# Kernel tuning notes

Measured on AMD Instinct MI355X. Metric: run time of the kernel, lower is better.

## Reference

```python
import jax, jax.numpy as jnp
import numpy as np

B, NN, F, H = 8, 1024, 256, 8
D = F // H
SCALE = D ** -0.5


def setup_inputs() -> dict:
    key = jax.random.key(0)
    ks = jax.random.split(key, 12)
    s = 0.02
    inp = {
        'ndata': jax.random.normal(ks[0], (B, NN, F), jnp.float32),
        'N': NN,
        'attn_bias': jax.random.normal(ks[1], (B, NN, NN, H), jnp.float32),
        'attn_mask': jax.random.randint(ks[2], (B, NN, NN), 0, 2).astype(bool),
        'Wq': jax.random.normal(ks[3], (F, F), jnp.float32) * s,
        'bq': jnp.zeros((F,), jnp.float32),
        'Wk': jax.random.normal(ks[4], (F, F), jnp.float32) * s,
        'bk': jnp.zeros((F,), jnp.float32),
        'Wv': jax.random.normal(ks[5], (F, F), jnp.float32) * s,
        'bv': jnp.zeros((F,), jnp.float32),
        'Wo': jax.random.normal(ks[6], (F, F), jnp.float32) * s,
        'bo': jnp.zeros((F,), jnp.float32),
    }
    return inp


def reference(ndata, N, attn_bias, attn_mask, Wq, bq, Wk, bk, Wv, bv, Wo, bo):
    b, n, f = ndata.shape
    # QKV projections (torch nn.Linear: x @ W.T + b), split heads
    q = (ndata @ Wq.T + bq).reshape(b, n, H, D) * SCALE
    k = (ndata @ Wk.T + bk).reshape(b, n, H, D)
    v = (ndata @ Wv.T + bv).reshape(b, n, H, D)
    # scores: (b, q, k, h) matching torch layout after its transposes
    scores = jnp.einsum('bqhd,bkhd->bqkh', q, k)
    scores = scores + attn_bias  # additive bias
    # original code force-unmasks column 0 so every row has a valid entry
    mask = attn_mask.at[:, :, 0].set(False)
    scores = jnp.where(mask[..., None], -jnp.inf, scores)
    attn = jax.nn.softmax(scores, axis=2)  # softmax over keys
    out = jnp.einsum('bqkh,bkhd->bqhd', attn, v).reshape(b, n, f)
    return out @ Wo.T + bo
```

## Files before the change

### kernel.cpp

```cpp
#include <hip/hip_runtime.h>
#include <hip/hip_bf16.h>

typedef __attribute__((ext_vector_type(8))) short short8;
typedef __attribute__((ext_vector_type(4))) float f32x4;

#define MFMA16(a,b,c) __builtin_amdgcn_mfma_f32_16x16x32_bf16((a),(b),(c),0,0,0)

static __device__ __forceinline__ unsigned int f2bf(float f){
    unsigned int u = __float_as_uint(f);
    u += 0x7FFFu + ((u >> 16) & 1u);
    return u >> 16;
}

static __device__ __forceinline__ short8 pack8(float4 a, float4 b){
    short8 r;
    r[0]=(short)f2bf(a.x); r[1]=(short)f2bf(a.y);
    r[2]=(short)f2bf(a.z); r[3]=(short)f2bf(a.w);
    r[4]=(short)f2bf(b.x); r[5]=(short)f2bf(b.y);
    r[6]=(short)f2bf(b.z); r[7]=(short)f2bf(b.w);
    return r;
}

__global__ __launch_bounds__(256) void mask_prep_k(
    const unsigned int* __restrict__ m, unsigned int* __restrict__ bmout)
{
    __shared__ int any_hi;
    const int tid  = threadIdx.x;
    const int lane = tid & 63;
    const unsigned int gbase = blockIdx.x*256u + tid;
    if (tid == 0) any_hi = 0;

    unsigned int wv[8]; unsigned int acc = 0;
    #pragma unroll
    for (int it = 0; it < 8; ++it){
        wv[it] = m[it*262144u + gbase];
        acc |= wv[it];
    }
    __syncthreads();
    if (acc & 0xFFFFFF00u) atomicOr(&any_hi, 1);
    __syncthreads();

    if (any_hi == 0){
        for (int it = 0; it < 32; ++it){
            unsigned int idx = it*262144u + gbase;
            unsigned int v = m[idx];
            unsigned long long bal = __ballot(v != 0u);
            if (lane == 0)
                *(unsigned long long*)(bmout + (idx >> 5)) = bal;
        }
    } else {
        #pragma unroll
        for (int it = 0; it < 8; ++it){
            unsigned int idx = it*262144u + gbase;
            unsigned int v = wv[it];
            unsigned int nib = (v | (v>>7) | (v>>14) | (v>>21)) & 0xFu;
            unsigned int x = nib << ((lane & 7)*4);
            x |= (unsigned int)__shfl_xor((int)x, 1);
            x |= (unsigned int)__shfl_xor((int)x, 2);
            x |= (unsigned int)__shfl_xor((int)x, 4);
            if ((lane & 7) == 0)
                bmout[idx >> 3] = x;
        }
    }
}

__global__ __launch_bounds__(256) void qkv_proj_k(
    const float* __restrict__ nd,
    const float* __restrict__ Wqp, const float* __restrict__ bqp,
    const float* __restrict__ Wkp, const float* __restrict__ bkp,
    const float* __restrict__ Wvp, const float* __restrict__ bvp,
    unsigned short* __restrict__ qout, unsigned short* __restrict__ kout,
    unsigned short* __restrict__ vtout)
{
    __shared__ __align__(16) unsigned short xl[64*264];
    const int tid  = threadIdx.x;
    const int bi   = blockIdx.x;
    const int kind = bi >> 7;
    const int R0   = (bi & 127) * 64;
    const int b    = R0 >> 10;
    const int n0   = R0 & 1023;

    #pragma unroll
    for (int it = 0; it < 16; ++it){
        int f4 = it*256 + tid;
        int r = f4 >> 6, c4 = f4 & 63;
        float4 v = *(const float4*)(nd + (size_t)(R0+r)*256 + c4*4);
        unsigned int lo = f2bf(v.x) | (f2bf(v.y) << 16);
        unsigned int hi = f2bf(v.z) | (f2bf(v.w) << 16);
        *(uint2*)&xl[r*264 + c4*4] = make_uint2(lo, hi);
    }
    __syncthreads();

    const int lane = tid & 63;
    const int w  = tid >> 6;
    const int ln = lane & 15;
    const int g  = lane >> 4;
    const int ow = w * 64;

    f32x4 acc[4][4];
    #pragma unroll
    for (int a=0;a<4;++a){
        #pragma unroll
        for (int c=0;c<4;++c) acc[a][c] = (f32x4){0.f,0.f,0.f,0.f};
    }

    if (kind < 2){
        const float* W  = kind ? Wkp : Wqp;
        const float* bb = kind ? bkp : bqp;
        unsigned short* op = kind ? kout : qout;
        const float scl = kind ? 1.0f : 0.17677669529663687f;
        for (int kk = 0; kk < 8; ++kk){
            short8 wf[4], xf[4];
            #pragma unroll
            for (int ot=0; ot<4; ++ot){
                const float* wp = W + (size_t)(ow + ot*16 + ln)*256 + kk*32 + g*8;
                wf[ot] = pack8(*(const float4*)wp, *(const float4*)(wp+4));
            }
            #pragma unroll
            for (int nt=0; nt<4; ++nt)
                xf[nt] = *(const short8*)&xl[(nt*16+ln)*264 + kk*32 + g*8];
            #pragma unroll
            for (int ot=0; ot<4; ++ot){
                #pragma unroll
                for (int nt=0; nt<4; ++nt)
                    acc[ot][nt] = MFMA16(wf[ot], xf[nt], acc[ot][nt]);
            }
        }
        #pragma unroll
        for (int ot=0; ot<4; ++ot){
            int o0 = ow + ot*16 + g*4;
            int h = o0 >> 5, d0 = o0 & 31;
            float4 b4 = *(const float4*)(bb + o0);
            #pragma unroll
            for (int nt=0; nt<4; ++nt){
                int n = n0 + nt*16 + ln;
                unsigned int lo = f2bf((acc[ot][nt][0]+b4.x)*scl) | (f2bf((acc[ot][nt][1]+b4.y)*scl)<<16);
                unsigned int hi = f2bf((acc[ot][nt][2]+b4.z)*scl) | (f2bf((acc[ot][nt][3]+b4.w)*scl)<<16);
                *(uint2*)(op + ((size_t)(b*8+h)*1024 + n)*32 + d0) = make_uint2(lo,hi);
            }
        }
    } else {
        for (int kk = 0; kk < 8; ++kk){
            short8 wf[4], xf[4];
            #pragma unroll
            for (int ot=0; ot<4; ++ot){
                const float* wp = Wvp + (size_t)(ow + ot*16 + ln)*256 + kk*32 + g*8;
                wf[ot] = pack8(*(const float4*)wp, *(const float4*)(wp+4));
            }
            #pragma unroll
            for (int nt=0; nt<4; ++nt)
                xf[nt] = *(const short8*)&xl[(nt*16+ln)*264 + kk*32 + g*8];
            #pragma unroll
            for (int nt=0; nt<4; ++nt){
                #pragma unroll
                for (int ot=0; ot<4; ++ot)
                    acc[nt][ot] = MFMA16(xf[nt], wf[ot], acc[nt][ot]);
            }
        }
        #pragma unroll
        for (int nt=0; nt<4; ++nt){
            int nb = n0 + nt*16 + g*4;
            #pragma unroll
            for (int ot=0; ot<4; ++ot){
                int o = ow + ot*16 + ln;
                int h = o >> 5, d = o & 31;
                float bvv = bvp[o];
                unsigned int lo = f2bf(acc[nt][ot][0]+bvv) | (f2bf(acc[nt][ot][1]+bvv)<<16);
                unsigned int hi = f2bf(acc[nt][ot][2]+bvv) | (f2bf(acc[nt][ot][3]+bvv)<<16);
                *(uint2*)(vtout + ((size_t)(b*8+h)*32 + d)*1024 + nb) = make_uint2(lo,hi);
            }
        }
    }
}

__global__ __launch_bounds__(256, 4) void attn_k(
    const unsigned short* __restrict__ qbuf, const unsigned short* __restrict__ kbuf,
    const unsigned short* __restrict__ vtbuf, const float* __restrict__ bias,
    const unsigned int* __restrict__ bm, unsigned short* __restrict__ ab)
{
    __shared__ __align__(16) float bs[4352];
    const int tid  = threadIdx.x;
    const int bi   = blockIdx.x;
    const int hh   = bi >> 9;
    const int b    = (bi >> 6) & 7;
    const int q0   = (bi & 63) * 16;
    const int lane = tid & 63;
    const int w    = tid >> 6;
    const int ln   = lane & 15;
    const int g    = lane >> 4;
    const int h    = hh*4 + w;

    const short8 qf = *(const short8*)(qbuf + ((size_t)(b*8+h)*1024 + q0 + ln)*32 + g*8);

    const int kperm = ((ln >> 2) << 3) + (ln & 3);
    const unsigned short* kp = kbuf  + ((size_t)(b*8+h)*1024 + kperm)*32 + g*8;
    const unsigned short* vp = vtbuf + ((size_t)(b*8+h)*32   + ln)*1024 + g*8;
    const unsigned int*  bmp = bm + (size_t)(b*1024 + q0 + ln)*32;

    const int sq  = tid >> 4;
    const int sk  = tid & 15;
    const float* bgp = bias + (size_t)(b*1024 + q0 + sq)*8192 + sk*8 + hh*4;
    const int hqb = sq*68;
    const int rb0 = w*1088 + ln*68 + 8*g;

    f32x4 acc0 = (f32x4){0.f,0.f,0.f,0.f};
    f32x4 acc1 = (f32x4){0.f,0.f,0.f,0.f};
    float lsum = 0.f;
    const f32x4 z4 = {0.f,0.f,0.f,0.f};

    float4 br0, br1, br2, br3;
    short8 kn0, kn1, kn2, kn3;
    unsigned int bm0, bm1;

#define LOAD_ALL(cc) do { int c_ = (cc); \
    br0 = *(const float4*)(bgp + (size_t)c_*512); \
    br1 = *(const float4*)(bgp + (size_t)c_*512 + 128); \
    br2 = *(const float4*)(bgp + (size_t)c_*512 + 256); \
    br3 = *(const float4*)(bgp + (size_t)c_*512 + 384); \
    kn0 = *(const short8*)(kp + c_*2048); \
    kn1 = *(const short8*)(kp + c_*2048 + 128); \
    kn2 = *(const short8*)(kp + c_*2048 + 1024); \
    kn3 = *(const short8*)(kp + c_*2048 + 1152); \
    bm0 = bmp[2*c_]; bm1 = bmp[2*c_+1]; } while(0)

#define STAGE1(R, IT) do { int kw_ = hqb + (IT)*16 + sk; \
    bs[kw_       ] = R.x; \
    bs[kw_ + 1088] = R.y; \
    bs[kw_ + 2176] = R.z; \
    bs[kw_ + 3264] = R.w; } while(0)

#define CHUNK_HALF(K0, K1, BMW, KH, VOFF) do { \
    f32x4 s0 = MFMA16(K0, qf, z4);    \
    f32x4 s1 = MFMA16(K1, qf, z4);    \
    f32x4 blo = *(const f32x4*)&bs[rb0 + (KH)*32]; \
    f32x4 bhi = *(const f32x4*)&bs[rb0 + (KH)*32 + 4]; \
    short8 vf0 = *(const short8*)(vp + (VOFF)); \
    short8 vf1 = *(const short8*)(vp + (VOFF) + 16*1024); \
    unsigned int mb_ = (BMW) >> (g*8); \
    float e0 = __expf(s0[0] + blo[0]); e0 = ((mb_>>0)&1u) ? 0.f : e0; \
    float e1 = __expf(s0[1] + blo[1]); e1 = ((mb_>>1)&1u) ? 0.f : e1; \
    float e2 = __expf(s0[2] + blo[2]); e2 = ((mb_>>2)&1u) ? 0.f : e2; \
    float e3 = __expf(s0[3] + blo[3]); e3 = ((mb_>>3)&1u) ? 0.f : e3; \
    float e4 = __expf(s1[0] + bhi[0]); e4 = ((mb_>>4)&1u) ? 0.f : e4; \
    float e5 = __expf(s1[1] + bhi[1]); e5 = ((mb_>>5)&1u) ? 0.f : e5; \
    float e6 = __expf(s1[2] + bhi[2]); e6 = ((mb_>>6)&1u) ? 0.f : e6; \
    float e7 = __expf(s1[3] + bhi[3]); e7 = ((mb_>>7)&1u) ? 0.f : e7; \
    lsum += ((e0+e1)+(e2+e3)) + ((e4+e5)+(e6+e7)); \
    int4 pw_ = make_int4( \
        (int)(f2bf(e0) | (f2bf(e1)<<16)), (int)(f2bf(e2) | (f2bf(e3)<<16)), \
        (int)(f2bf(e4) | (f2bf(e5)<<16)), (int)(f2bf(e6) | (f2bf(e7)<<16))); \
    short8 pf_ = *(short8*)&pw_; \
    acc0 = MFMA16(vf0, pf_, acc0); \
    acc1 = MFMA16(vf1, pf_, acc1); } while(0)

    LOAD_ALL(0);
    bm0 &= ~1u;

    #pragma unroll 1
    for (int cc = 0; cc < 16; ++cc){
        STAGE1(br0, 0); STAGE1(br1, 1); STAGE1(br2, 2); STAGE1(br3, 3);
        short8 ck0 = kn0, ck1 = kn1, ck2 = kn2, ck3 = kn3;
        unsigned int cb0 = bm0, cb1 = bm1;
        if (cc + 1 < 16) LOAD_ALL(cc + 1);
        __syncthreads();

        CHUNK_HALF(ck0, ck1, cb0, 0, cc*64);
        CHUNK_HALF(ck2, ck3, cb1, 1, cc*64 + 32);
        __syncthreads();
    }

    float ps = lsum;
    ps += __shfl_xor(ps, 16);
    ps += __shfl_xor(ps, 32);
    float inv = 1.0f / ps;
    {
        int n = q0 + ln;
        unsigned int lo0 = f2bf(acc0[0]*inv) | (f2bf(acc0[1]*inv)<<16);
        unsigned int hi0 = f2bf(acc0[2]*inv) | (f2bf(acc0[3]*inv)<<16);
        *(uint2*)(ab + ((size_t)(b*1024 + n))*256 + h*32 + g*4) = make_uint2(lo0,hi0);
        unsigned int lo1 = f2bf(acc1[0]*inv) | (f2bf(acc1[1]*inv)<<16);
        unsigned int hi1 = f2bf(acc1[2]*inv) | (f2bf(acc1[3]*inv)<<16);
        *(uint2*)(ab + ((size_t)(b*1024 + n))*256 + h*32 + 16 + g*4) = make_uint2(lo1,hi1);
    }
#undef LOAD_ALL
#undef STAGE1
#undef CHUNK_HALF
}

__global__ __launch_bounds__(256) void oproj_k(
    const unsigned short* __restrict__ ab, const float* __restrict__ Wop,
    const float* __restrict__ bop, float* __restrict__ out)
{
    __shared__ __align__(16) unsigned short al[32*264];
    const int tid = threadIdx.x;
    const int R0 = blockIdx.x * 32;
    #pragma unroll
    for (int it=0; it<4; ++it){
        int f8 = it*256 + tid;
        int r = f8 >> 5, c8 = f8 & 31;
        *(short8*)&al[r*264 + c8*8] = *(const short8*)(ab + (size_t)(R0+r)*256 + c8*8);
    }
    __syncthreads();
    const int lane = tid & 63;
    const int w = tid >> 6, ln = lane & 15, g = lane >> 4;
    const int ow = w*64;
    f32x4 acc[4][2];
    #pragma unroll
    for (int a=0;a<4;++a){ acc[a][0]=(f32x4){0.f,0.f,0.f,0.f}; acc[a][1]=(f32x4){0.f,0.f,0.f,0.f}; }
    for (int kk=0;kk<8;++kk){
        short8 wf[4], xf[2];
        #pragma unroll
        for (int ot=0;ot<4;++ot){
            const float* wp = Wop + (size_t)(ow+ot*16+ln)*256 + kk*32 + g*8;
            wf[ot] = pack8(*(const float4*)wp, *(const float4*)(wp+4));
        }
        #pragma unroll
        for (int nt=0;nt<2;++nt)
            xf[nt] = *(const short8*)&al[(nt*16+ln)*264 + kk*32 + g*8];
        #pragma unroll
        for (int ot=0;ot<4;++ot){
            #pragma unroll
            for (int nt=0;nt<2;++nt)
                acc[ot][nt] = MFMA16(wf[ot], xf[nt], acc[ot][nt]);
        }
    }
    #pragma unroll
    for (int ot=0;ot<4;++ot){
        int o0 = ow + ot*16 + g*4;
        float4 b4 = *(const float4*)(bop + o0);
        #pragma unroll
        for (int nt=0;nt<2;++nt){
            int n = R0 + nt*16 + ln;
            float4 res;
            res.x = acc[ot][nt][0] + b4.x;
            res.y = acc[ot][nt][1] + b4.y;
            res.z = acc[ot][nt][2] + b4.z;
            res.w = acc[ot][nt][3] + b4.w;
            *(float4*)(out + (size_t)n*256 + o0) = res;
        }
    }
}

extern "C" void kernel_launch(void* const* d_in, const int* in_sizes, int n_in,
                              void* d_out, int out_size, void* d_ws, size_t ws_size,
                              hipStream_t stream)
{
    (void)in_sizes; (void)n_in; (void)out_size; (void)ws_size;
    const float* nd   = (const float*)d_in[0];
    const float* bias = (const float*)d_in[2];
    const int* mask   = (const int*)d_in[3];
    const float* Wq = (const float*)d_in[4];
    const float* bq = (const float*)d_in[5];
    const float* Wk = (const float*)d_in[6];
    const float* bk = (const float*)d_in[7];
    const float* Wv = (const float*)d_in[8];
    const float* bv = (const float*)d_in[9];
    const float* Wo = (const float*)d_in[10];
    const float* bo = (const float*)d_in[11];
    float* out = (float*)d_out;

    const size_t ELEMS = (size_t)8*8*1024*32;
    unsigned short* qb  = (unsigned short*)d_ws;
    unsigned short* kb  = qb  + ELEMS;
    unsigned short* vtb = kb  + ELEMS;
    unsigned short* ab  = vtb + ELEMS;
    unsigned int* bmw   = (unsigned int*)(ab + ELEMS);

    mask_prep_k<<<1024, 256, 0, stream>>>((const unsigned int*)mask, bmw);
    qkv_proj_k<<<384, 256, 0, stream>>>(nd, Wq, bq, Wk, bk, Wv, bv, qb, kb, vtb);
    attn_k<<<1024, 256, 0, stream>>>(qb, kb, vtb, bias, bmw, ab);
    oproj_k<<<256, 256, 0, stream>>>(ab, Wo, bo, out);
}
```

Before: 163.3 us.

## Split attention over key halves with all heads per block and combine kernel

The attention grid now splits the key dimension into two halves instead of splitting heads into two groups. Each block covers all 8 heads (two per wave) for one half of the keys, so bias rows are read as contiguous 256-float spans. Unnormalised partial outputs and row sums go to fp32 workspace, and a new combine kernel adds the two halves, normalises and writes bf16. This aims to improve bias load coalescing and per-wave MFMA work, at the cost of extra global traffic for the partials and one more kernel launch.

```diff
diff --git a/kernel.cpp b/kernel.cpp
--- a/kernel.cpp
+++ b/kernel.cpp
@@ -176,66 +176,73 @@
 __global__ __launch_bounds__(256, 4) void attn_k(
     const unsigned short* __restrict__ qbuf, const unsigned short* __restrict__ kbuf,
     const unsigned short* __restrict__ vtbuf, const float* __restrict__ bias,
-    const unsigned int* __restrict__ bm, unsigned short* __restrict__ ab)
-{
-    __shared__ __align__(16) float bs[4352];
+    const unsigned int* __restrict__ bm, float* __restrict__ opart,
+    float* __restrict__ lpart)
+{
+    __shared__ __align__(16) float bs[4608];
     const int tid  = threadIdx.x;
     const int bi   = blockIdx.x;
-    const int hh   = bi >> 9;
+    const int kq   = bi >> 9;
     const int b    = (bi >> 6) & 7;
     const int q0   = (bi & 63) * 16;
     const int lane = tid & 63;
     const int w    = tid >> 6;
     const int ln   = lane & 15;
     const int g    = lane >> 4;
-    const int h    = hh*4 + w;
-
-    const short8 qf = *(const short8*)(qbuf + ((size_t)(b*8+h)*1024 + q0 + ln)*32 + g*8);
+    const int h0   = 2*w, h1 = 2*w + 1;
+
+    const short8 qf0 = *(const short8*)(qbuf + ((size_t)(b*8+h0)*1024 + q0 + ln)*32 + g*8);
+    const short8 qf1 = *(const short8*)(qbuf + ((size_t)(b*8+h1)*1024 + q0 + ln)*32 + g*8);
 
     const int kperm = ((ln >> 2) << 3) + (ln & 3);
-    const unsigned short* kp = kbuf  + ((size_t)(b*8+h)*1024 + kperm)*32 + g*8;
-    const unsigned short* vp = vtbuf + ((size_t)(b*8+h)*32   + ln)*1024 + g*8;
+    const unsigned short* kpA = kbuf + ((size_t)(b*8+h0)*1024 + kperm)*32 + g*8;
+    const unsigned short* kpB = kbuf + ((size_t)(b*8+h1)*1024 + kperm)*32 + g*8;
+    const unsigned short* vpA = vtbuf + ((size_t)(b*8+h0)*32 + ln)*1024 + g*8;
+    const unsigned short* vpB = vtbuf + ((size_t)(b*8+h1)*32 + ln)*1024 + g*8;
     const unsigned int*  bmp = bm + (size_t)(b*1024 + q0 + ln)*32;
 
     const int sq  = tid >> 4;
-    const int sk  = tid & 15;
-    const float* bgp = bias + (size_t)(b*1024 + q0 + sq)*8192 + sk*8 + hh*4;
-    const int hqb = sq*68;
-    const int rb0 = w*1088 + ln*68 + 8*g;
-
-    f32x4 acc0 = (f32x4){0.f,0.f,0.f,0.f};
-    f32x4 acc1 = (f32x4){0.f,0.f,0.f,0.f};
-    float lsum = 0.f;
+    const float* bgp = bias + (size_t)(b*1024 + q0 + sq)*8192 + (tid & 15)*4;
+    const int hqb = (tid & 1)*4*576 + sq*36;
+    const int kpw = (tid & 15) >> 1;
+    const int rb0 = h0*576 + ln*36 + 8*g;
+    const int rb1 = rb0 + 576;
+
+    f32x4 acc00 = (f32x4){0.f,0.f,0.f,0.f};
+    f32x4 acc01 = (f32x4){0.f,0.f,0.f,0.f};
+    f32x4 acc10 = (f32x4){0.f,0.f,0.f,0.f};
+    f32x4 acc11 = (f32x4){0.f,0.f,0.f,0.f};
+    float lsum0 = 0.f, lsum1 = 0.f;
     const f32x4 z4 = {0.f,0.f,0.f,0.f};
 
     float4 br0, br1, br2, br3;
-    short8 kn0, kn1, kn2, kn3;
-    unsigned int bm0, bm1;
+    short8 knA0, knA1, knB0, knB1;
+    unsigned int bm0;
 
 #define LOAD_ALL(cc) do { int c_ = (cc); \
-    br0 = *(const float4*)(bgp + (size_t)c_*512); \
-    br1 = *(const float4*)(bgp + (size_t)c_*512 + 128); \
-    br2 = *(const float4*)(bgp + (size_t)c_*512 + 256); \
-    br3 = *(const float4*)(bgp + (size_t)c_*512 + 384); \
-    kn0 = *(const short8*)(kp + c_*2048); \
-    kn1 = *(const short8*)(kp + c_*2048 + 128); \
-    kn2 = *(const short8*)(kp + c_*2048 + 1024); \
-    kn3 = *(const short8*)(kp + c_*2048 + 1152); \
-    bm0 = bmp[2*c_]; bm1 = bmp[2*c_+1]; } while(0)
-
-#define STAGE1(R, IT) do { int kw_ = hqb + (IT)*16 + sk; \
-    bs[kw_       ] = R.x; \
-    bs[kw_ + 1088] = R.y; \
-    bs[kw_ + 2176] = R.z; \
-    bs[kw_ + 3264] = R.w; } while(0)
-
-#define CHUNK_HALF(K0, K1, BMW, KH, VOFF) do { \
-    f32x4 s0 = MFMA16(K0, qf, z4);    \
-    f32x4 s1 = MFMA16(K1, qf, z4);    \
-    f32x4 blo = *(const f32x4*)&bs[rb0 + (KH)*32]; \
-    f32x4 bhi = *(const f32x4*)&bs[rb0 + (KH)*32 + 4]; \
-    short8 vf0 = *(const short8*)(vp + (VOFF)); \
-    short8 vf1 = *(const short8*)(vp + (VOFF) + 16*1024); \
+    br0 = *(const float4*)(bgp + (size_t)c_*256); \
+    br1 = *(const float4*)(bgp + (size_t)c_*256 + 64); \
+    br2 = *(const float4*)(bgp + (size_t)c_*256 + 128); \
+    br3 = *(const float4*)(bgp + (size_t)c_*256 + 192); \
+    knA0 = *(const short8*)(kpA + c_*1024); \
+    knA1 = *(const short8*)(kpA + c_*1024 + 128); \
+    knB0 = *(const short8*)(kpB + c_*1024); \
+    knB1 = *(const short8*)(kpB + c_*1024 + 128); \
+    bm0 = bmp[c_]; } while(0)
+
+#define STAGE1(R, IT) do { int kw_ = (IT)*8 + kpw; \
+    bs[hqb        + kw_] = R.x; \
+    bs[hqb +  576 + kw_] = R.y; \
+    bs[hqb + 1152 + kw_] = R.z; \
+    bs[hqb + 1728 + kw_] = R.w; } while(0)
+
+#define CHUNK32(K0, K1, QF, RB, VP, VOFF, BMW, ACCL, ACCH, LSUM) do { \
+    f32x4 s0 = MFMA16(K0, QF, z4);    \
+    f32x4 s1 = MFMA16(K1, QF, z4);    \
+    f32x4 blo = *(const f32x4*)&bs[RB]; \
+    f32x4 bhi = *(const f32x4*)&bs[RB + 4]; \
+    short8 vf0 = *(const short8*)(VP + (VOFF)); \
+    short8 vf1 = *(const short8*)(VP + (VOFF) + 16*1024); \
     unsigned int mb_ = (BMW) >> (g*8); \
     float e0 = __expf(s0[0] + blo[0]); e0 = ((mb_>>0)&1u) ? 0.f : e0; \
     float e1 = __expf(s0[1] + blo[1]); e1 = ((mb_>>1)&1u) ? 0.f : e1; \
@@ -245,46 +252,68 @@
     float e5 = __expf(s1[1] + bhi[1]); e5 = ((mb_>>5)&1u) ? 0.f : e5; \
     float e6 = __expf(s1[2] + bhi[2]); e6 = ((mb_>>6)&1u) ? 0.f : e6; \
     float e7 = __expf(s1[3] + bhi[3]); e7 = ((mb_>>7)&1u) ? 0.f : e7; \
-    lsum += ((e0+e1)+(e2+e3)) + ((e4+e5)+(e6+e7)); \
+    LSUM += ((e0+e1)+(e2+e3)) + ((e4+e5)+(e6+e7)); \
     int4 pw_ = make_int4( \
         (int)(f2bf(e0) | (f2bf(e1)<<16)), (int)(f2bf(e2) | (f2bf(e3)<<16)), \
         (int)(f2bf(e4) | (f2bf(e5)<<16)), (int)(f2bf(e6) | (f2bf(e7)<<16))); \
     short8 pf_ = *(short8*)&pw_; \
-    acc0 = MFMA16(vf0, pf_, acc0); \
-    acc1 = MFMA16(vf1, pf_, acc1); } while(0)
-
-    LOAD_ALL(0);
-    bm0 &= ~1u;
+    ACCL = MFMA16(vf0, pf_, ACCL); \
+    ACCH = MFMA16(vf1, pf_, ACCH); } while(0)
+
+    LOAD_ALL(kq*16);
+    if (kq == 0) bm0 &= ~1u;
 
     #pragma unroll 1
     for (int cc = 0; cc < 16; ++cc){
+        const int c = kq*16 + cc;
         STAGE1(br0, 0); STAGE1(br1, 1); STAGE1(br2, 2); STAGE1(br3, 3);
-        short8 ck0 = kn0, ck1 = kn1, ck2 = kn2, ck3 = kn3;
-        unsigned int cb0 = bm0, cb1 = bm1;
-        if (cc + 1 < 16) LOAD_ALL(cc + 1);
+        short8 cA0 = knA0, cA1 = knA1, cB0 = knB0, cB1 = knB1;
+        unsigned int cb = bm0;
+        if (cc + 1 < 16) LOAD_ALL(c + 1);
         __syncthreads();
 
-        CHUNK_HALF(ck0, ck1, cb0, 0, cc*64);
-        CHUNK_HALF(ck2, ck3, cb1, 1, cc*64 + 32);
+        CHUNK32(cA0, cA1, qf0, rb0, vpA, c*32, cb, acc00, acc01, lsum0);
+        CHUNK32(cB0, cB1, qf1, rb1, vpB, c*32, cb, acc10, acc11, lsum1);
         __syncthreads();
     }
 
-    float ps = lsum;
-    ps += __shfl_xor(ps, 16);
-    ps += __shfl_xor(ps, 32);
-    float inv = 1.0f / ps;
-    {
-        int n = q0 + ln;
-        unsigned int lo0 = f2bf(acc0[0]*inv) | (f2bf(acc0[1]*inv)<<16);
-        unsigned int hi0 = f2bf(acc0[2]*inv) | (f2bf(acc0[3]*inv)<<16);
-        *(uint2*)(ab + ((size_t)(b*1024 + n))*256 + h*32 + g*4) = make_uint2(lo0,hi0);
-        unsigned int lo1 = f2bf(acc1[0]*inv) | (f2bf(acc1[1]*inv)<<16);
-        unsigned int hi1 = f2bf(acc1[2]*inv) | (f2bf(acc1[3]*inv)<<16);
-        *(uint2*)(ab + ((size_t)(b*1024 + n))*256 + h*32 + 16 + g*4) = make_uint2(lo1,hi1);
+    #pragma unroll
+    for (int h2 = 0; h2 < 2; ++h2){
+        float ps = h2 ? lsum1 : lsum0;
+        ps += __shfl_xor(ps, 16);
+        ps += __shfl_xor(ps, 32);
+        size_t row = ((size_t)(kq*8 + b)*1024 + q0 + ln)*8 + (2*w + h2);
+        if (g == 0) lpart[row] = ps;
+        float* ob = opart + row*32;
+        f32x4 aL = h2 ? acc10 : acc00;
+        f32x4 aH = h2 ? acc11 : acc01;
+        *(float4*)(ob + g*4)      = make_float4(aL[0], aL[1], aL[2], aL[3]);
+        *(float4*)(ob + 16 + g*4) = make_float4(aH[0], aH[1], aH[2], aH[3]);
     }
 #undef LOAD_ALL
 #undef STAGE1
-#undef CHUNK_HALF
+#undef CHUNK32
+}
+
+__global__ __launch_bounds__(256) void combine_k(
+    const float* __restrict__ op, const float* __restrict__ lp,
+    unsigned short* __restrict__ ab)
+{
+    const size_t STR = (size_t)8*1024*8*32;
+    int idx = blockIdx.x*256 + threadIdx.x;
+    size_t off = (size_t)idx * 4;
+    float4 s0 = *(const float4*)(op + off);
+    float4 s1 = *(const float4*)(op + STR + off);
+    int bqh = idx >> 3;
+    float l = lp[bqh] + lp[65536 + bqh];
+    float inv = 1.0f / l;
+    float rx = (s0.x + s1.x) * inv;
+    float ry = (s0.y + s1.y) * inv;
+    float rz = (s0.z + s1.z) * inv;
+    float rw = (s0.w + s1.w) * inv;
+    unsigned int lo = f2bf(rx) | (f2bf(ry) << 16);
+    unsigned int hi = f2bf(rz) | (f2bf(rw) << 16);
+    *(uint2*)(ab + off) = make_uint2(lo, hi);
 }
 
 __global__ __launch_bounds__(256) void oproj_k(
@@ -365,9 +394,12 @@
     unsigned short* vtb = kb  + ELEMS;
     unsigned short* ab  = vtb + ELEMS;
     unsigned int* bmw   = (unsigned int*)(ab + ELEMS);
+    float* opart        = (float*)(bmw + 262144);
+    float* lpart        = opart + (size_t)2*ELEMS;
 
     mask_prep_k<<<1024, 256, 0, stream>>>((const unsigned int*)mask, bmw);
     qkv_proj_k<<<384, 256, 0, stream>>>(nd, Wq, bq, Wk, bk, Wv, bv, qb, kb, vtb);
-    attn_k<<<1024, 256, 0, stream>>>(qb, kb, vtb, bias, bmw, ab);
+    attn_k<<<1024, 256, 0, stream>>>(qb, kb, vtb, bias, bmw, opart, lpart);
+    combine_k<<<2048, 256, 0, stream>>>(opart, lpart, ab);
     oproj_k<<<256, 256, 0, stream>>>(ab, Wo, bo, out);
 }
```

New measurement: 146.9 us. -10.0%, faster.
